# Kernel optimization log

Measured on AMD Instinct MI355X. Metric: run time of the kernel, lower is better.

Reference implementation:

```python
import jax, jax.numpy as jnp
import numpy as np

NUM_NEIGHBORS = 16
HIDDEN = 64
FEAT = 64


def setup_inputs() -> dict:
    key = jax.random.key(0)
    ks = jax.random.split(key, 16)
    B, S, N = 1, 4, 4096

    def dense(k, fan_in, fan_out):
        # variance_scaling(2.0, fan_in, truncated_normal) ~ normal with std sqrt(2/fan_in)
        w = jax.random.truncated_normal(k, -2.0, 2.0, (fan_in, fan_out), jnp.float32)
        return w * jnp.sqrt(2.0 / fan_in) / 0.87962566

    inp = {
        "x": jax.random.normal(ks[0], (B, S, N, FEAT), jnp.float32),
        "pos": jax.random.uniform(ks[1], (B, S, N, 3), jnp.float32),
        "Wq": dense(ks[2], FEAT, HIDDEN), "bq": jnp.zeros((HIDDEN,), jnp.float32),
        "Wk": dense(ks[3], FEAT, HIDDEN), "bk": jnp.zeros((HIDDEN,), jnp.float32),
        "Wv": dense(ks[4], FEAT, HIDDEN), "bv": jnp.zeros((HIDDEN,), jnp.float32),
        "Wpe": dense(ks[5], 3, HIDDEN), "bpe": jnp.zeros((HIDDEN,), jnp.float32),
        "Wpd": dense(ks[6], 3, HIDDEN), "bpd": jnp.zeros((HIDDEN,), jnp.float32),
        "Wa": dense(ks[7], HIDDEN, 1), "ba": jnp.zeros((1,), jnp.float32),
        "Wo": dense(ks[8], HIDDEN, FEAT), "bo": jnp.zeros((FEAT,), jnp.float32),
    }
    return inp


def reference(x, pos, Wq, bq, Wk, bk, Wv, bv, Wpe, bpe, Wpd, bpd, Wa, ba, Wo, bo):
    # x: [B,S,N,F], pos: [B,S,N,3]
    q = x @ Wq + bq                      # [B,S,N,H]
    k = x @ Wk + bk
    v = x @ Wv + bv
    pos_enc = pos @ Wpe + bpe            # [B,S,N,H]

    # pairwise squared distances: diff[n,m] = pos[n] - pos[m]
    pos_diff = pos[..., :, None, :] - pos[..., None, :, :]   # [B,S,N,N,3]
    dist = jnp.sum(pos_diff ** 2, axis=-1)                   # [B,S,N,N]
    _, neighbor_idx = jax.lax.top_k(-dist, NUM_NEIGHBORS)    # [B,S,N,K]

    def gather_neighbors(a):
        # a: [B,S,N,C] -> [B,S,N,K,C]
        return jnp.take_along_axis(a[:, :, None, :, :], neighbor_idx[..., None], axis=3)

    k_neighbors = gather_neighbors(k)          # [B,S,N,K,H]
    v_neighbors = gather_neighbors(v)
    p_neighbors = gather_neighbors(pos_enc)
    pos_rel = gather_neighbors(pos) - pos[..., None, :]      # [B,S,N,K,3]
    pos_diff_enc = pos_rel @ Wpd + bpd                       # [B,S,N,K,H]

    q = (q + pos_enc)[..., None, :]                          # [B,S,N,1,H]
    scale = jnp.sqrt(jnp.float32(HIDDEN))
    attn = q * (k_neighbors + p_neighbors + pos_diff_enc) / scale  # [B,S,N,K,H]
    attn = (attn @ Wa + ba).squeeze(-1)                      # [B,S,N,K]
    attn = jax.nn.softmax(attn, axis=-1)
    out = jnp.einsum('bsnk,bsnkh->bsnh', attn, v_neighbors)  # [B,S,N,H]
    out = jax.nn.gelu(out @ Wo + bo)                          # [B,S,N,F]
    return x + out
```

## Files before the change

kernel.cpp:

```cpp
#include <hip/hip_runtime.h>
#include <hip/hip_bf16.h>

#define S_DIM 4
#define N_PTS 4096
#define P_TOT (S_DIM * N_PTS)
#define KNB 16

#define GD 16
#define NCELL (GD * GD * GD)
#define CSTRIDE (NCELL + 1)
#define CAP 224
#define MAXRUN 256
#define PROJ_BLKS 256

__global__ __launch_bounds__(1024) void pre_kernel(
    const float* __restrict__ x, const float* __restrict__ pos,
    const float* __restrict__ Wq, const float* __restrict__ bq,
    const float* __restrict__ Wk, const float* __restrict__ bk,
    const float* __restrict__ Wv, const float* __restrict__ bv,
    const float* __restrict__ Wpe, const float* __restrict__ bpe,
    float* __restrict__ qpe, float* __restrict__ kpe, float* __restrict__ vout,
    int* __restrict__ cell_start, float4* __restrict__ gpts)
{
    int tid = threadIdx.x;

    if (blockIdx.x < PROJ_BLKS) {
        __shared__ float xs[64][64];
        __shared__ float psf[192];
        int h = tid & 63;
        int wv = tid >> 6;
        int g0 = blockIdx.x * 64;

        ((float4*)xs)[tid] = ((const float4*)(x + (size_t)g0 * 64))[tid];
        if (tid < 48)
            ((float4*)psf)[tid] = ((const float4*)(pos + (size_t)g0 * 3))[tid];
        __syncthreads();

        int pbase = wv * 4;
        float aq[4], ak[4], av[4];
        #pragma unroll
        for (int p = 0; p < 4; ++p) { aq[p] = bq[h]; ak[p] = bk[h]; av[p] = bv[h]; }

        #pragma unroll 8
        for (int f = 0; f < 64; ++f) {
            float wq = Wq[f * 64 + h];
            float wk = Wk[f * 64 + h];
            float wvv = Wv[f * 64 + h];
            #pragma unroll
            for (int p = 0; p < 4; ++p) {
                float xf = xs[pbase + p][f];
                aq[p] = fmaf(xf, wq, aq[p]);
                ak[p] = fmaf(xf, wk, ak[p]);
                av[p] = fmaf(xf, wvv, av[p]);
            }
        }

        float wpe0 = Wpe[0 * 64 + h], wpe1 = Wpe[1 * 64 + h], wpe2 = Wpe[2 * 64 + h];
        float bpeh = bpe[h];
        #pragma unroll
        for (int p = 0; p < 4; ++p) {
            int pp = pbase + p;
            float pe = fmaf(psf[pp * 3 + 0], wpe0,
                       fmaf(psf[pp * 3 + 1], wpe1,
                       fmaf(psf[pp * 3 + 2], wpe2, bpeh)));
            int gp = g0 + pp;
            qpe[gp * 64 + h]  = aq[p] + pe;
            kpe[gp * 64 + h]  = ak[p] + pe;
            vout[gp * 64 + h] = av[p];
        }
    } else {
        __shared__ int cnt[NCELL];
        __shared__ int start[NCELL + 1];
        __shared__ int wtot[16];

        int s = blockIdx.x - PROJ_BLKS;
        const float* psrc = pos + (size_t)s * N_PTS * 3;

        for (int i = tid; i < NCELL; i += 1024) cnt[i] = 0;
        __syncthreads();

        const float4* g4 = (const float4*)psrc;
        float4 a = g4[tid * 3 + 0];
        float4 b = g4[tid * 3 + 1];
        float4 c4 = g4[tid * 3 + 2];
        float xx[4] = {a.x, a.w, b.z, c4.y};
        float yy[4] = {a.y, b.x, b.w, c4.z};
        float zz[4] = {a.z, b.y, c4.x, c4.w};
        int cell[4];
        #pragma unroll
        for (int k = 0; k < 4; ++k) {
            int cx = min(GD - 1, max(0, (int)(xx[k] * 16.0f)));
            int cy = min(GD - 1, max(0, (int)(yy[k] * 16.0f)));
            int cz = min(GD - 1, max(0, (int)(zz[k] * 16.0f)));
            cell[k] = (cx * GD + cy) * GD + cz;
            atomicAdd(&cnt[cell[k]], 1);
        }
        __syncthreads();

        int wv = tid >> 6, lane = tid & 63;
        int c0 = cnt[tid * 4 + 0], c1 = cnt[tid * 4 + 1];
        int c2 = cnt[tid * 4 + 2], c3 = cnt[tid * 4 + 3];
        int ts = c0 + c1 + c2 + c3;
        int inc = ts;
        #pragma unroll
        for (int off = 1; off < 64; off <<= 1) {
            int n = __shfl_up(inc, off, 64);
            if (lane >= off) inc += n;
        }
        if (lane == 63) wtot[wv] = inc;
        __syncthreads();
        if (wv == 0) {
            int v0 = (lane < 16) ? wtot[lane] : 0;
            int i2 = v0;
            #pragma unroll
            for (int off = 1; off < 16; off <<= 1) {
                int n = __shfl_up(i2, off, 64);
                if (lane >= off) i2 += n;
            }
            if (lane < 16) wtot[lane] = i2 - v0;
        }
        __syncthreads();
        int base = wtot[wv] + inc - ts;
        start[tid * 4 + 0] = base;
        start[tid * 4 + 1] = base + c0;
        start[tid * 4 + 2] = base + c0 + c1;
        start[tid * 4 + 3] = base + c0 + c1 + c2;
        if (tid == 0) start[NCELL] = N_PTS;
        __syncthreads();

        for (int i = tid; i < NCELL + 1; i += 1024)
            cell_start[s * CSTRIDE + i] = start[i];
        for (int i = tid; i < NCELL; i += 1024) cnt[i] = 0;
        __syncthreads();

        #pragma unroll
        for (int k = 0; k < 4; ++k) {
            int slot = start[cell[k]] + atomicAdd(&cnt[cell[k]], 1);
            gpts[(size_t)s * N_PTS + slot] =
                make_float4(xx[k], yy[k], zz[k],
                            __uint_as_float((unsigned)(tid * 4 + k)));
        }
    }
}

__device__ __forceinline__ float readlane_f(float v, int lane) {
    return __uint_as_float(__builtin_amdgcn_readlane(__float_as_uint(v), lane));
}

__global__ __launch_bounds__(512) void knn_attn_kernel(
    const float* __restrict__ x, const float* __restrict__ pos,
    const int* __restrict__ cell_start, const float4* __restrict__ gpts,
    const float* __restrict__ Wpd, const float* __restrict__ bpd,
    const float* __restrict__ Wa, const float* __restrict__ ba,
    const float* __restrict__ Wo, const float* __restrict__ bo,
    const float* __restrict__ qpe, const float* __restrict__ kpe,
    const float* __restrict__ v, float* __restrict__ out)
{
    __shared__ unsigned long long buf[8][CAP];
    __shared__ int Ptab[8][MAXRUN + 1];
    __shared__ int LOtab[8][MAXRUN];
    __shared__ int ridx[8][KNB];
    __shared__ float ohs[8][64];

    int tid = threadIdx.x;
    int wave = tid >> 6, lane = tid & 63;

    int bid = blockIdx.x;
    int swz = (bid & 7) * 256 + (bid >> 3);
    int qslot = swz * 8 + wave;
    int s = qslot >> 12;
    int sbase = s << 12;
    const int* cs = cell_start + s * CSTRIDE;
    const float4* gp = gpts + (size_t)sbase;
    unsigned long long* mybuf = buf[wave];
    int* Pw = Ptab[wave];
    int* Lw = LOtab[wave];

    float4 q4 = gp[qslot & (N_PTS - 1)];
    float qx = q4.x, qy = q4.y, qz = q4.z;
    int g = sbase + (int)__float_as_uint(q4.w);

    float bx = fminf(qx, 1.f - qx), by = fminf(qy, 1.f - qy), bz = fminf(qz, 1.f - qz);
    float r = 0.125f;
    #pragma unroll
    for (int it = 0; it < 2; ++it) {
        float ux = fminf(bx / r, 1.f), uy = fminf(by / r, 1.f), uz = fminf(bz / r, 1.f);
        float fx = 0.5f + 0.75f * ux - 0.25f * ux * ux * ux;
        float fy = 0.5f + 0.75f * uy - 0.25f * uy * uy * uy;
        float fz = 0.5f + 0.75f * uz - 0.25f * uz * uz * uz;
        float est = 17157.3f * r * r * r * fx * fy * fz;
        float sc = exp2f(0.3333333f * log2f(40.f / est));
        r = fminf(fmaxf(r * sc, 0.09f), 0.32f);
    }
    r = __uint_as_float(__builtin_amdgcn_readfirstlane(__float_as_uint(r)));

    unsigned long long lanemask_lt = (lane == 0) ? 0ull : (~0ull >> (64 - lane));

    int cnt = 0;
    for (int tries = 0; tries < 6; ++tries) {
        float B = r * r;
        float Bc = B * 1.0002f + 1e-7f;
        int xlo = max(0, (int)floorf((qx - r) * 16.f - 1e-4f));
        int xhi = min(GD - 1, (int)floorf((qx + r) * 16.f + 1e-4f));
        int ylo = max(0, (int)floorf((qy - r) * 16.f - 1e-4f));
        int yhi = min(GD - 1, (int)floorf((qy + r) * 16.f + 1e-4f));
        int nx = xhi - xlo + 1, ny = yhi - ylo + 1;
        int NC = __builtin_amdgcn_readfirstlane(nx * ny);
        float rcp_ny = 1.f / (float)ny;

        int carry = 0;
        for (int c0 = 0; c0 < NC; c0 += 64) {
            int cidx = c0 + lane;
            bool vld = cidx < NC;
            int qd = (int)(((float)cidx + 0.5f) * rcp_ny);
            int iy = ylo + (cidx - qd * ny);
            int ix = xlo + qd;
            float x0 = (float)ix * 0.0625f;
            float ax = fmaxf(0.f, fmaxf(x0 - qx, qx - (x0 + 0.0625f)));
            float y0 = (float)iy * 0.0625f;
            float ay = fmaxf(0.f, fmaxf(y0 - qy, qy - (y0 + 0.0625f)));
            float rem = Bc - ax * ax - ay * ay;
            int lo = 0, len = 0;
            if (vld && rem > 0.f) {
                float zs = sqrtf(rem) + 1e-4f;
                int zl = max(0, (int)floorf((qz - zs) * 16.f));
                int zh = min(GD - 1, (int)floorf((qz + zs) * 16.f));
                int cb = (ix * GD + iy) * GD;
                lo = cs[cb + zl];
                len = cs[cb + zh + 1] - lo;
            }
            int inc = len;
            #pragma unroll
            for (int off = 1; off < 64; off <<= 1) {
                int n = __shfl_up(inc, off, 64);
                if (lane >= off) inc += n;
            }
            int excl = carry + inc - len;
            if (vld) { Pw[cidx] = excl; Lw[cidx] = lo - excl; }
            carry += __builtin_amdgcn_readlane(inc, 63);
        }
        if (lane == 0) Pw[NC] = carry;
        int T = carry;
        __builtin_amdgcn_wave_barrier();
        asm volatile("s_waitcnt lgkmcnt(0)" ::: "memory");

        cnt = 0;
        for (int p0 = 0; p0 < T; p0 += 64) {
            int pidx = p0 + lane;
            bool act = pidx < T;
            int blo = 0, bhi = NC;
            #pragma unroll
            for (int bs = 0; bs < 8; ++bs) {
                int mid = (blo + bhi) >> 1;
                int pm = Pw[mid];
                bool cge = pidx >= pm;
                blo = cge ? mid : blo;
                bhi = cge ? bhi : mid;
            }
            int src = act ? (Lw[blo] + pidx) : 0;
            float4 p = gp[src];
            float dx = qx - p.x, dy = qy - p.y, dz = qz - p.z;
            float d = fmaf(dx, dx, fmaf(dy, dy, dz * dz));
            bool pred = act && (d < B);
            unsigned long long m = __ballot(pred);
            if (pred) {
                int slot = cnt + __popcll(m & lanemask_lt);
                if (slot < CAP)
                    mybuf[slot] =
                        ((unsigned long long)__float_as_uint(d) << 32) |
                        (unsigned long long)__float_as_uint(p.w);
            }
            cnt += __popcll(m);
        }
        if (cnt >= KNB && cnt <= CAP) break;
        r = (cnt < KNB) ? r * 1.35f : r * 0.72f;
    }
    cnt = min(cnt, CAP);

    __builtin_amdgcn_wave_barrier();
    asm volatile("s_waitcnt lgkmcnt(0)" ::: "memory");

    if (lane < KNB) ridx[wave][lane] = 0;
    for (int bb = 0; bb < cnt; bb += 64) {
        int slot = bb + lane;
        unsigned long long my = (slot < cnt) ? mybuf[slot] : ~0ull;
        int rank = 0;
        for (int j = 0; j < cnt; ++j)
            rank += (mybuf[j] < my) ? 1 : 0;
        if (slot < cnt && rank < KNB)
            ridx[wave][rank] = (int)(unsigned)(my & 0xFFFFFFFFull);
    }
    __builtin_amdgcn_wave_barrier();
    asm volatile("s_waitcnt lgkmcnt(0)" ::: "memory");
    int res = (lane < KNB) ? ridx[wave][lane] : 0;

    int h = lane;
    float qv = qpe[g * 64 + h];
    float wh = qv * Wa[h] * 0.125f;

    float wpd0 = Wpd[0 * 64 + h], wpd1 = Wpd[1 * 64 + h], wpd2 = Wpd[2 * 64 + h];
    float bpdh = bpd[h];

    int jidx[KNB];
    float t[KNB];
    #pragma unroll
    for (int k = 0; k < KNB; ++k) {
        int jj = sbase + __builtin_amdgcn_readlane(res, k);
        jidx[k] = jj;
        float rx = pos[jj * 3 + 0] - qx;
        float ry = pos[jj * 3 + 1] - qy;
        float rz = pos[jj * 3 + 2] - qz;
        float pd = fmaf(rx, wpd0, fmaf(ry, wpd1, fmaf(rz, wpd2, bpdh)));
        t[k] = wh * (kpe[jj * 64 + h] + pd);
    }

    #pragma unroll
    for (int kk = 0; kk < 8; ++kk) {
        float a = t[2 * kk]     + __shfl_xor(t[2 * kk],     32, 64);
        float b = t[2 * kk + 1] + __shfl_xor(t[2 * kk + 1], 32, 64);
        t[kk] = (h & 32) ? b : a;
    }
    #pragma unroll
    for (int kk = 0; kk < 4; ++kk) {
        float a = t[2 * kk]     + __shfl_xor(t[2 * kk],     16, 64);
        float b = t[2 * kk + 1] + __shfl_xor(t[2 * kk + 1], 16, 64);
        t[kk] = (h & 16) ? b : a;
    }
    #pragma unroll
    for (int kk = 0; kk < 2; ++kk) {
        float a = t[2 * kk]     + __shfl_xor(t[2 * kk],     8, 64);
        float b = t[2 * kk + 1] + __shfl_xor(t[2 * kk + 1], 8, 64);
        t[kk] = (h & 8) ? b : a;
    }
    {
        float a = t[0] + __shfl_xor(t[0], 4, 64);
        float b = t[1] + __shfl_xor(t[1], 4, 64);
        t[0] = (h & 4) ? b : a;
    }
    float rr = t[0];
    rr += __shfl_xor(rr, 2, 64);
    rr += __shfl_xor(rr, 1, 64);

    float lg = rr + ba[0];
    float mx = lg;
    mx = fmaxf(mx, __shfl_xor(mx, 4, 64));
    mx = fmaxf(mx, __shfl_xor(mx, 8, 64));
    mx = fmaxf(mx, __shfl_xor(mx, 16, 64));
    mx = fmaxf(mx, __shfl_xor(mx, 32, 64));
    float e = expf(lg - mx);
    float sm = e;
    sm += __shfl_xor(sm, 4, 64);
    sm += __shfl_xor(sm, 8, 64);
    sm += __shfl_xor(sm, 16, 64);
    sm += __shfl_xor(sm, 32, 64);
    float wk_mine = e * (1.0f / sm);

    const int rev[KNB] = {0, 8, 4, 12, 2, 10, 6, 14, 1, 9, 5, 13, 3, 11, 7, 15};
    float oh = 0.f;
    #pragma unroll
    for (int k = 0; k < KNB; ++k) {
        float wk = readlane_f(wk_mine, rev[k] << 2);
        oh = fmaf(wk, v[jidx[k] * 64 + h], oh);
    }

    ohs[wave][h] = oh;
    __builtin_amdgcn_wave_barrier();
    asm volatile("s_waitcnt lgkmcnt(0)" ::: "memory");
    const float4* oh4 = (const float4*)ohs[wave];
    float yy0 = bo[h], yy1 = 0.f;
    #pragma unroll
    for (int i = 0; i < 16; ++i) {
        float4 o = oh4[i];
        yy0 = fmaf(o.x, Wo[(4 * i + 0) * 64 + h], yy0);
        yy1 = fmaf(o.y, Wo[(4 * i + 1) * 64 + h], yy1);
        yy0 = fmaf(o.z, Wo[(4 * i + 2) * 64 + h], yy0);
        yy1 = fmaf(o.w, Wo[(4 * i + 3) * 64 + h], yy1);
    }
    float y = yy0 + yy1;

    float t3 = y + 0.044715f * y * y * y;
    float ge = 0.5f * y * (1.0f + tanhf(0.7978845608028654f * t3));

    out[g * 64 + h] = x[g * 64 + h] + ge;
}

extern "C" void kernel_launch(void* const* d_in, const int* in_sizes, int n_in,
                              void* d_out, int out_size, void* d_ws, size_t ws_size,
                              hipStream_t stream) {
    const float* x   = (const float*)d_in[0];
    const float* pos = (const float*)d_in[1];
    const float* Wq  = (const float*)d_in[2];
    const float* bq  = (const float*)d_in[3];
    const float* Wk  = (const float*)d_in[4];
    const float* bk  = (const float*)d_in[5];
    const float* Wv  = (const float*)d_in[6];
    const float* bv  = (const float*)d_in[7];
    const float* Wpe = (const float*)d_in[8];
    const float* bpe = (const float*)d_in[9];
    const float* Wpd = (const float*)d_in[10];
    const float* bpd = (const float*)d_in[11];
    const float* Wa  = (const float*)d_in[12];
    const float* ba  = (const float*)d_in[13];
    const float* Wo  = (const float*)d_in[14];
    const float* bo  = (const float*)d_in[15];
    float* out = (float*)d_out;

    float* ws  = (float*)d_ws;
    float* qpe = ws;
    float* kpe = ws + (size_t)P_TOT * 64;
    float* vv  = ws + (size_t)2 * P_TOT * 64;
    int*   cstart = (int*)(ws + (size_t)3 * P_TOT * 64);
    float4* gpts = (float4*)(cstart + S_DIM * CSTRIDE);

    pre_kernel<<<PROJ_BLKS + S_DIM, 1024, 0, stream>>>(
        x, pos, Wq, bq, Wk, bk, Wv, bv, Wpe, bpe, qpe, kpe, vv, cstart, gpts);
    knn_attn_kernel<<<P_TOT / 8, 512, 0, stream>>>(
        x, pos, cstart, gpts, Wpd, bpd, Wa, ba, Wo, bo, qpe, kpe, vv, out);
}
```

Before: 59.99 us.

## Replace per-candidate binary search with explicit index map; hoist per-query loads

The prefix-sum table of cell runs, which each candidate lane searched with an 8-step binary search, is replaced by a per-wave ushort map in LDS. Each lane writes the point indices of its run directly into that map, so the candidate loop becomes a single LDS lookup. The map holds at most 512 candidates, and larger radii are shrunk and retried. Per-query and weight loads (qpe, x, Wa, bo, Wpd, bpd, ba) are hoisted to the kernel start so their latency overlaps the search, and the initial radius target drops from 40 to 32 expected points to cut scan work. The serial per-lane map writes may diverge, and the smaller radius may trigger more retries.

```diff
diff --git a/kernel.cpp b/kernel.cpp
--- a/kernel.cpp
+++ b/kernel.cpp
@@ -10,7 +10,7 @@
 #define NCELL (GD * GD * GD)
 #define CSTRIDE (NCELL + 1)
 #define CAP 224
-#define MAXRUN 256
+#define MAPSZ 512
 #define PROJ_BLKS 256
 
 __global__ __launch_bounds__(1024) void pre_kernel(
@@ -157,8 +157,7 @@
     const float* __restrict__ v, float* __restrict__ out)
 {
     __shared__ unsigned long long buf[8][CAP];
-    __shared__ int Ptab[8][MAXRUN + 1];
-    __shared__ int LOtab[8][MAXRUN];
+    __shared__ unsigned short map[8][MAPSZ];
     __shared__ int ridx[8][KNB];
     __shared__ float ohs[8][64];
 
@@ -173,12 +172,19 @@
     const int* cs = cell_start + s * CSTRIDE;
     const float4* gp = gpts + (size_t)sbase;
     unsigned long long* mybuf = buf[wave];
-    int* Pw = Ptab[wave];
-    int* Lw = LOtab[wave];
+    unsigned short* mymap = map[wave];
 
     float4 q4 = gp[qslot & (N_PTS - 1)];
     float qx = q4.x, qy = q4.y, qz = q4.z;
     int g = sbase + (int)__float_as_uint(q4.w);
+
+    float qv   = qpe[g * 64 + lane];
+    float xres = x[g * 64 + lane];
+    float wa   = Wa[lane];
+    float boh  = bo[lane];
+    float bpdh = bpd[lane];
+    float wpd0 = Wpd[0 * 64 + lane], wpd1 = Wpd[1 * 64 + lane], wpd2 = Wpd[2 * 64 + lane];
+    float ba0  = ba[0];
 
     float bx = fminf(qx, 1.f - qx), by = fminf(qy, 1.f - qy), bz = fminf(qz, 1.f - qz);
     float r = 0.125f;
@@ -189,7 +195,7 @@
         float fy = 0.5f + 0.75f * uy - 0.25f * uy * uy * uy;
         float fz = 0.5f + 0.75f * uz - 0.25f * uz * uz * uz;
         float est = 17157.3f * r * r * r * fx * fy * fz;
-        float sc = exp2f(0.3333333f * log2f(40.f / est));
+        float sc = exp2f(0.3333333f * log2f(32.f / est));
         r = fminf(fmaxf(r * sc, 0.09f), 0.32f);
     }
     r = __uint_as_float(__builtin_amdgcn_readfirstlane(__float_as_uint(r)));
@@ -207,6 +213,9 @@
         int nx = xhi - xlo + 1, ny = yhi - ylo + 1;
         int NC = __builtin_amdgcn_readfirstlane(nx * ny);
         float rcp_ny = 1.f / (float)ny;
+
+        __builtin_amdgcn_wave_barrier();
+        asm volatile("s_waitcnt lgkmcnt(0)" ::: "memory");
 
         int carry = 0;
         for (int c0 = 0; c0 < NC; c0 += 64) {
@@ -236,11 +245,15 @@
                 if (lane >= off) inc += n;
             }
             int excl = carry + inc - len;
-            if (vld) { Pw[cidx] = excl; Lw[cidx] = lo - excl; }
+            for (int i = 0; i < len; ++i) {
+                int d = excl + i;
+                if (d < MAPSZ) mymap[d] = (unsigned short)(lo + i);
+            }
             carry += __builtin_amdgcn_readlane(inc, 63);
         }
-        if (lane == 0) Pw[NC] = carry;
         int T = carry;
+        if (T > MAPSZ) { r = r * 0.72f; continue; }
+
         __builtin_amdgcn_wave_barrier();
         asm volatile("s_waitcnt lgkmcnt(0)" ::: "memory");
 
@@ -248,16 +261,7 @@
         for (int p0 = 0; p0 < T; p0 += 64) {
             int pidx = p0 + lane;
             bool act = pidx < T;
-            int blo = 0, bhi = NC;
-            #pragma unroll
-            for (int bs = 0; bs < 8; ++bs) {
-                int mid = (blo + bhi) >> 1;
-                int pm = Pw[mid];
-                bool cge = pidx >= pm;
-                blo = cge ? mid : blo;
-                bhi = cge ? bhi : mid;
-            }
-            int src = act ? (Lw[blo] + pidx) : 0;
+            int src = mymap[act ? pidx : 0];
             float4 p = gp[src];
             float dx = qx - p.x, dy = qy - p.y, dz = qz - p.z;
             float d = fmaf(dx, dx, fmaf(dy, dy, dz * dz));
@@ -295,11 +299,7 @@
     int res = (lane < KNB) ? ridx[wave][lane] : 0;
 
     int h = lane;
-    float qv = qpe[g * 64 + h];
-    float wh = qv * Wa[h] * 0.125f;
-
-    float wpd0 = Wpd[0 * 64 + h], wpd1 = Wpd[1 * 64 + h], wpd2 = Wpd[2 * 64 + h];
-    float bpdh = bpd[h];
+    float wh = qv * wa * 0.125f;
 
     int jidx[KNB];
     float t[KNB];
@@ -341,7 +341,7 @@
     rr += __shfl_xor(rr, 2, 64);
     rr += __shfl_xor(rr, 1, 64);
 
-    float lg = rr + ba[0];
+    float lg = rr + ba0;
     float mx = lg;
     mx = fmaxf(mx, __shfl_xor(mx, 4, 64));
     mx = fmaxf(mx, __shfl_xor(mx, 8, 64));
@@ -367,7 +367,7 @@
     __builtin_amdgcn_wave_barrier();
     asm volatile("s_waitcnt lgkmcnt(0)" ::: "memory");
     const float4* oh4 = (const float4*)ohs[wave];
-    float yy0 = bo[h], yy1 = 0.f;
+    float yy0 = boh, yy1 = 0.f;
     #pragma unroll
     for (int i = 0; i < 16; ++i) {
         float4 o = oh4[i];
@@ -381,7 +381,7 @@
     float t3 = y + 0.044715f * y * y * y;
     float ge = 0.5f * y * (1.0f + tanhf(0.7978845608028654f * t3));
 
-    out[g * 64 + h] = x[g * 64 + h] + ge;
+    out[g * 64 + h] = xres + ge;
 }
 
 extern "C" void kernel_launch(void* const* d_in, const int* in_sizes, int n_in,
```

Result: no change. 60.66 us (+1.1%).
